# Kernel optimization log

Hardware: AMD Instinct MI355X
Metric: run time of the kernel (lower is better)

The kernel has to match this reference:

```python
import jax, jax.numpy as jnp
import numpy as np

B, L, D, Y = 8, 2500, 512, 8921


def setup_inputs() -> dict:
    key = jax.random.key(0)
    k1, k2, k3, k4, k5, k6 = jax.random.split(key, 6)
    x = jax.random.normal(k1, (B, L, D), dtype=jnp.float32)
    target = jax.random.uniform(k2, (B, Y), dtype=jnp.float32)
    text_inputs = jax.random.randint(k3, (B, L), 0, 50000, dtype=jnp.int32)
    # Xavier-uniform-like init for the two [Y, D] weights
    lim = float(np.sqrt(6.0 / (Y + D)))
    U_weight = jax.random.uniform(k4, (Y, D), dtype=jnp.float32, minval=-lim, maxval=lim)
    final_weight = jax.random.uniform(k5, (Y, D), dtype=jnp.float32, minval=-lim, maxval=lim)
    final_bias = jax.random.uniform(k6, (Y,), dtype=jnp.float32, minval=-0.05, maxval=0.05)
    return {"x": x, "target": target, "text_inputs": text_inputs,
            "U_weight": U_weight, "final_weight": final_weight, "final_bias": final_bias}


def reference(x, target, text_inputs, U_weight, final_weight, final_bias):
    # att: [B, Y, L] = U.weight @ x^T
    att = jnp.einsum('yd,bld->byl', U_weight, x)
    # softmax over sequence dim
    alpha = jax.nn.softmax(att, axis=2)
    # per-label context: [B, Y, D]
    m = jnp.einsum('byl,bld->byd', alpha, x)
    # gated reduction instead of a linear layer: [B, Y]
    y = jnp.einsum('byd,yd->by', m, final_weight) + final_bias
    # BCEWithLogitsLoss (mean over all elements), numerically stable
    loss = jnp.mean(jnp.maximum(y, 0.0) - y * target + jnp.log1p(jnp.exp(-jnp.abs(y))))
    return (y, loss)
```

## Files before the change

### kernel.cpp

```cpp
#include <hip/hip_runtime.h>
#include <stdint.h>

#define B_ 8
#define L_ 2500
#define D_ 512
#define Y_ 8921
#define LP 2560
#define YP 8960
#define BLK 128
#define BK 32
#define NKT 16
#define NS 4
#define LTS 5

typedef float f32x4 __attribute__((ext_vector_type(4)));
typedef __bf16 bf16x8 __attribute__((ext_vector_type(8)));
typedef unsigned short u16;
typedef unsigned int u32;

__device__ __forceinline__ u32 pack2(float a, float b) {
  u32 ua = __float_as_uint(a); ua = (ua + 0x7FFFu + ((ua >> 16) & 1u)) >> 16;
  u32 ub = __float_as_uint(b); ub = (ub + 0x7FFFu + ((ub >> 16) & 1u)) >> 16;
  return ua | (ub << 16);
}

__global__ void cvt_x_kernel(const float* __restrict__ x, u16* __restrict__ xb) {
  int idx = blockIdx.x * 256 + threadIdx.x;
  int row = idx >> 6;
  int c8  = (idx & 63) << 3;
  int b = row / LP;
  int l = row - b * LP;
  uint4 o;
  if (l < L_) {
    const float* s = x + (size_t)(b * L_ + l) * D_ + c8;
    float4 f0 = *(const float4*)s;
    float4 f1 = *(const float4*)(s + 4);
    o.x = pack2(f0.x, f0.y); o.y = pack2(f0.z, f0.w);
    o.z = pack2(f1.x, f1.y); o.w = pack2(f1.z, f1.w);
  } else {
    o = make_uint4(0u, 0u, 0u, 0u);
  }
  *(uint4*)(xb + (size_t)row * D_ + c8) = o;
}

__global__ void cvt_w_kernel(const float* __restrict__ U, const float* __restrict__ Wf,
                             u16* __restrict__ Ub, u16* __restrict__ Wb) {
  int idx = blockIdx.x * 256 + threadIdx.x;
  const int half = YP * 64;
  const float* src = U; u16* dst = Ub;
  int i = idx;
  if (idx >= half) { i -= half; src = Wf; dst = Wb; }
  int row = i >> 6;
  int c8  = (i & 63) << 3;
  uint4 o;
  if (row < Y_) {
    const float* s = src + (size_t)row * D_ + c8;
    float4 f0 = *(const float4*)s;
    float4 f1 = *(const float4*)(s + 4);
    o.x = pack2(f0.x, f0.y); o.y = pack2(f0.z, f0.w);
    o.z = pack2(f1.x, f1.y); o.w = pack2(f1.z, f1.w);
  } else {
    o = make_uint4(0u, 0u, 0u, 0u);
  }
  *(uint4*)(dst + (size_t)row * D_ + c8) = o;
}

__device__ __forceinline__ void async16(const u16* g, u16* l) {
  __builtin_amdgcn_global_load_lds(
      (const __attribute__((address_space(1))) u32*)g,
      (__attribute__((address_space(3))) u32*)l, 16, 0, 0);
}

__global__ __launch_bounds__(256, 2) void fused_kernel(
    const u16* __restrict__ xb,
    const u16* __restrict__ Ub,
    const u16* __restrict__ Wb,
    float* __restrict__ part)
{
  __shared__ __align__(16) u16 sU[BLK * BK];
  __shared__ __align__(16) u16 sW[BLK * BK];
  __shared__ __align__(16) u16 sX[BLK * BK];

  const int t    = threadIdx.x;
  const int lane = t & 63;
  const int wv   = t >> 6;
  const int l16  = lane & 15;
  const int q    = lane >> 4;
  const int b    = blockIdx.y;
  const int y0   = blockIdx.x * BLK;
  const int s    = blockIdx.z;

  const int srow = t >> 2;
  const int scol = (t & 3) << 3;
  const u16* gU0 = Ub + (size_t)(y0 + srow) * D_ + scol;
  const u16* gU1 = gU0 + (size_t)64 * D_;
  const u16* gW0 = Wb + (size_t)(y0 + srow) * D_ + scol;
  const u16* gW1 = gW0 + (size_t)64 * D_;
  const u16* gXb = xb + (size_t)b * LP * D_ + (size_t)srow * D_ + scol;
  u16* lU0 = sU + t * 8;  u16* lU1 = sU + 2048 + t * 8;
  u16* lW0 = sW + t * 8;  u16* lW1 = sW + 2048 + t * 8;
  u16* lX0 = sX + t * 8;  u16* lX1 = sX + 2048 + t * 8;

  float M[8], Z[8], W[8];
#pragma unroll
  for (int i = 0; i < 8; ++i) { M[i] = -1e30f; Z[i] = 0.f; W[i] = 0.f; }

  const f32x4 z4 = {0.f, 0.f, 0.f, 0.f};

  for (int ltl = 0; ltl < LTS; ++ltl) {
    const int l0 = (s * LTS + ltl) * BLK;
    const u16* gX0 = gXb + (size_t)l0 * D_;
    const u16* gX1 = gX0 + (size_t)64 * D_;

    f32x4 accA[2][8], accS[2][8];
#pragma unroll
    for (int ry = 0; ry < 2; ++ry)
#pragma unroll
      for (int cl = 0; cl < 8; ++cl) { accA[ry][cl] = z4; accS[ry][cl] = z4; }

    for (int kt = 0; kt < NKT; ++kt) {
      const int ko = kt * BK;
      __syncthreads();
      async16(gU0 + ko, lU0);
      async16(gU1 + ko, lU1);
      async16(gW0 + ko, lW0);
      async16(gW1 + ko, lW1);
      async16(gX0 + ko, lX0);
      async16(gX1 + ko, lX1);
      __syncthreads();

      bf16x8 aU0 = *(const bf16x8*)(const void*)(sU + (wv * 32 + l16) * BK + q * 8);
      bf16x8 aU1 = *(const bf16x8*)(const void*)(sU + (wv * 32 + 16 + l16) * BK + q * 8);
      bf16x8 aW0 = *(const bf16x8*)(const void*)(sW + (wv * 32 + l16) * BK + q * 8);
      bf16x8 aW1 = *(const bf16x8*)(const void*)(sW + (wv * 32 + 16 + l16) * BK + q * 8);
#pragma unroll
      for (int cl = 0; cl < 8; ++cl) {
        bf16x8 bX = *(const bf16x8*)(const void*)(sX + (cl * 16 + l16) * BK + q * 8);
        accA[0][cl] = __builtin_amdgcn_mfma_f32_16x16x32_bf16(aU0, bX, accA[0][cl], 0, 0, 0);
        accA[1][cl] = __builtin_amdgcn_mfma_f32_16x16x32_bf16(aU1, bX, accA[1][cl], 0, 0, 0);
        accS[0][cl] = __builtin_amdgcn_mfma_f32_16x16x32_bf16(aW0, bX, accS[0][cl], 0, 0, 0);
        accS[1][cl] = __builtin_amdgcn_mfma_f32_16x16x32_bf16(aW1, bX, accS[1][cl], 0, 0, 0);
      }
    }

    const bool boundary = (l0 + BLK > L_);
#pragma unroll
    for (int ry = 0; ry < 2; ++ry) {
#pragma unroll
      for (int r = 0; r < 4; ++r) {
        const int si = ry * 4 + r;
        float a[8];
        if (boundary) {
#pragma unroll
          for (int cl = 0; cl < 8; ++cl) {
            float v = accA[ry][cl][r];
            a[cl] = (l0 + cl * 16 + l16 >= L_) ? -1e30f : v;
          }
        } else {
#pragma unroll
          for (int cl = 0; cl < 8; ++cl) a[cl] = accA[ry][cl][r];
        }
        float tmax = a[0];
#pragma unroll
        for (int cl = 1; cl < 8; ++cl) tmax = fmaxf(tmax, a[cl]);
        const float mnew  = fmaxf(M[si], tmax);
        const float scale = __expf(M[si] - mnew);
        float zl = 0.f, wl = 0.f;
#pragma unroll
        for (int cl = 0; cl < 8; ++cl) {
          float p = __expf(a[cl] - mnew);
          zl += p;
          wl = fmaf(p, accS[ry][cl][r], wl);
        }
        Z[si] = fmaf(Z[si], scale, zl);
        W[si] = fmaf(W[si], scale, wl);
        M[si] = mnew;
      }
    }
  }

#pragma unroll
  for (int si = 0; si < 8; ++si) {
    float M0 = M[si], Z0 = Z[si], W0 = W[si];
#pragma unroll
    for (int st = 1; st <= 8; st <<= 1) {
      const float Mo = __shfl_xor(M0, st);
      const float Zo = __shfl_xor(Z0, st);
      const float Wo = __shfl_xor(W0, st);
      const float mn = fmaxf(M0, Mo);
      const float sa = __expf(M0 - mn);
      const float sb = __expf(Mo - mn);
      Z0 = Z0 * sa + Zo * sb;
      W0 = W0 * sa + Wo * sb;
      M0 = mn;
    }
    M[si] = M0; Z[si] = Z0; W[si] = W0;
  }

  if (l16 == 0) {
    float* p = part + ((size_t)(b * 70 + blockIdx.x) * NS + s) * 384;
#pragma unroll
    for (int ry = 0; ry < 2; ++ry) {
#pragma unroll
      for (int r = 0; r < 4; ++r) {
        const int si = ry * 4 + r;
        const int yl = wv * 32 + ry * 16 + q * 4 + r;
        p[yl]       = M[si];
        p[128 + yl] = Z[si];
        p[256 + yl] = W[si];
      }
    }
  }
}

__global__ void combine_kernel(const float* __restrict__ part,
                               const float* __restrict__ bias,
                               const float* __restrict__ target,
                               float* __restrict__ out) {
  const int idx = blockIdx.x * 256 + threadIdx.x;
  float lpart = 0.f;
  if (idx < B_ * Y_) {
    const int b = idx / Y_;
    const int y = idx - b * Y_;
    const int yt = y >> 7, yl = y & 127;
    const float* p = part + ((size_t)(b * 70 + yt) * NS) * 384 + yl;
    float M = -1e30f;
#pragma unroll
    for (int s2 = 0; s2 < NS; ++s2) M = fmaxf(M, p[s2 * 384]);
    float Z = 0.f, W = 0.f;
#pragma unroll
    for (int s2 = 0; s2 < NS; ++s2) {
      const float e = __expf(p[s2 * 384] - M);
      Z = fmaf(p[s2 * 384 + 128], e, Z);
      W = fmaf(p[s2 * 384 + 256], e, W);
    }
    const float yv = W / Z + bias[y];
    out[idx] = yv;
    const float tg = target[idx];
    lpart = fmaxf(yv, 0.f) - yv * tg + log1pf(__expf(-fabsf(yv)));
  }
  lpart += __shfl_xor(lpart, 1);  lpart += __shfl_xor(lpart, 2);
  lpart += __shfl_xor(lpart, 4);  lpart += __shfl_xor(lpart, 8);
  lpart += __shfl_xor(lpart, 16); lpart += __shfl_xor(lpart, 32);
  if ((threadIdx.x & 63) == 0)
    atomicAdd(out + (size_t)B_ * Y_, lpart * (1.0f / (B_ * Y_)));
}

extern "C" void kernel_launch(void* const* d_in, const int* in_sizes, int n_in,
                              void* d_out, int out_size, void* d_ws, size_t ws_size,
                              hipStream_t stream) {
  const float* x      = (const float*)d_in[0];
  const float* target = (const float*)d_in[1];
  const float* U      = (const float*)d_in[3];
  const float* Wf     = (const float*)d_in[4];
  const float* bias   = (const float*)d_in[5];
  float* out = (float*)d_out;

  u16* xb = (u16*)d_ws;
  u16* Ub = xb + (size_t)B_ * LP * D_;
  u16* Wb = Ub + (size_t)YP * D_;
  float* part = (float*)(Wb + (size_t)YP * D_);

  hipMemsetAsync(out + (size_t)B_ * Y_, 0, sizeof(float), stream);
  cvt_x_kernel<<<dim3((B_ * LP * 64) / 256), 256, 0, stream>>>(x, xb);
  cvt_w_kernel<<<dim3((2 * YP * 64) / 256), 256, 0, stream>>>(U, Wf, Ub, Wb);
  fused_kernel<<<dim3(YP / BLK, B_, NS), 256, 0, stream>>>(xb, Ub, Wb, part);
  combine_kernel<<<dim3((B_ * Y_ + 255) / 256), 256, 0, stream>>>(part, bias, target, out);
}
```

Baseline: 568.8 us.

## Switch fused attention GEMMs from bf16 to block-scaled MX-FP8 MFMA

Measured after the change: 2.070 ms. 3.64x slower.

```diff
diff --git a/kernel.cpp b/kernel.cpp
--- a/kernel.cpp
+++ b/kernel.cpp
@@ -8,78 +8,98 @@
 #define LP 2560
 #define YP 8960
 #define BLK 128
-#define BK 32
-#define NKT 16
 #define NS 4
 #define LTS 5
 
 typedef float f32x4 __attribute__((ext_vector_type(4)));
-typedef __bf16 bf16x8 __attribute__((ext_vector_type(8)));
-typedef unsigned short u16;
+typedef int   v8i  __attribute__((ext_vector_type(8)));
 typedef unsigned int u32;
-
-__device__ __forceinline__ u32 pack2(float a, float b) {
-  u32 ua = __float_as_uint(a); ua = (ua + 0x7FFFu + ((ua >> 16) & 1u)) >> 16;
-  u32 ub = __float_as_uint(b); ub = (ub + 0x7FFFu + ((ub >> 16) & 1u)) >> 16;
-  return ua | (ub << 16);
-}
-
-__global__ void cvt_x_kernel(const float* __restrict__ x, u16* __restrict__ xb) {
-  int idx = blockIdx.x * 256 + threadIdx.x;
-  int row = idx >> 6;
-  int c8  = (idx & 63) << 3;
-  int b = row / LP;
-  int l = row - b * LP;
-  uint4 o;
-  if (l < L_) {
-    const float* s = x + (size_t)(b * L_ + l) * D_ + c8;
-    float4 f0 = *(const float4*)s;
-    float4 f1 = *(const float4*)(s + 4);
-    o.x = pack2(f0.x, f0.y); o.y = pack2(f0.z, f0.w);
-    o.z = pack2(f1.x, f1.y); o.w = pack2(f1.z, f1.w);
+typedef uint8_t u8;
+
+__device__ __forceinline__ void quant32(const float* __restrict__ src, bool valid,
+                                        u8* __restrict__ dst, u8* __restrict__ sdst) {
+  float v[32];
+  float amax = 0.f;
+  if (valid) {
+#pragma unroll
+    for (int j = 0; j < 8; ++j) {
+      float4 f = *(const float4*)(src + j * 4);
+      v[j * 4 + 0] = f.x; v[j * 4 + 1] = f.y; v[j * 4 + 2] = f.z; v[j * 4 + 3] = f.w;
+      amax = fmaxf(amax, fmaxf(fmaxf(fabsf(f.x), fabsf(f.y)), fmaxf(fabsf(f.z), fabsf(f.w))));
+    }
   } else {
-    o = make_uint4(0u, 0u, 0u, 0u);
-  }
-  *(uint4*)(xb + (size_t)row * D_ + c8) = o;
-}
-
-__global__ void cvt_w_kernel(const float* __restrict__ U, const float* __restrict__ Wf,
-                             u16* __restrict__ Ub, u16* __restrict__ Wb) {
-  int idx = blockIdx.x * 256 + threadIdx.x;
-  const int half = YP * 64;
-  const float* src = U; u16* dst = Ub;
-  int i = idx;
-  if (idx >= half) { i -= half; src = Wf; dst = Wb; }
-  int row = i >> 6;
-  int c8  = (i & 63) << 3;
-  uint4 o;
-  if (row < Y_) {
-    const float* s = src + (size_t)row * D_ + c8;
-    float4 f0 = *(const float4*)s;
-    float4 f1 = *(const float4*)(s + 4);
-    o.x = pack2(f0.x, f0.y); o.y = pack2(f0.z, f0.w);
-    o.z = pack2(f1.x, f1.y); o.w = pack2(f1.z, f1.w);
-  } else {
-    o = make_uint4(0u, 0u, 0u, 0u);
-  }
-  *(uint4*)(dst + (size_t)row * D_ + c8) = o;
-}
-
-__device__ __forceinline__ void async16(const u16* g, u16* l) {
+#pragma unroll
+    for (int j = 0; j < 32; ++j) v[j] = 0.f;
+  }
+  int e = 0;
+  float sinv = 1.f;
+  if (amax > 0.f) {
+    e = (int)ceilf(__log2f(amax) - 8.80735492206f);
+    e = max(-127, min(127, e));
+    sinv = exp2f((float)(-e));
+  }
+  u32 w[8];
+#pragma unroll
+  for (int j = 0; j < 8; ++j) {
+    u32 r = __builtin_amdgcn_cvt_pk_fp8_f32(v[j * 4 + 0] * sinv, v[j * 4 + 1] * sinv, 0, false);
+    r = __builtin_amdgcn_cvt_pk_fp8_f32(v[j * 4 + 2] * sinv, v[j * 4 + 3] * sinv, r, true);
+    w[j] = r;
+  }
+  *(uint4*)dst        = make_uint4(w[0], w[1], w[2], w[3]);
+  *(uint4*)(dst + 16) = make_uint4(w[4], w[5], w[6], w[7]);
+  *sdst = (u8)(e + 127);
+}
+
+__global__ void cvt_x8(const float* __restrict__ x, u8* __restrict__ xb, u8* __restrict__ xs) {
+  int gid = blockIdx.x * 256 + threadIdx.x;
+  int row = gid >> 4, blk = gid & 15;
+  int b = row / LP, l = row - b * LP;
+  bool valid = (l < L_);
+  const float* src = x + (size_t)(b * L_ + l) * D_ + blk * 32;
+  quant32(src, valid, xb + (size_t)row * 512 + blk * 32, xs + (size_t)row * 16 + blk);
+}
+
+__global__ void cvt_w8(const float* __restrict__ U, const float* __restrict__ Wf,
+                       u8* __restrict__ Ub, u8* __restrict__ Us,
+                       u8* __restrict__ Wb, u8* __restrict__ Ws) {
+  int gid = blockIdx.x * 256 + threadIdx.x;
+  const int half = YP * 16;
+  const float* src = U; u8* db = Ub; u8* ds = Us;
+  int i = gid;
+  if (gid >= half) { i -= half; src = Wf; db = Wb; ds = Ws; }
+  int row = i >> 4, blk = i & 15;
+  bool valid = (row < Y_);
+  quant32(src + (size_t)row * D_ + blk * 32, valid,
+          db + (size_t)row * 512 + blk * 32, ds + (size_t)row * 16 + blk);
+}
+
+__device__ __forceinline__ void async16b(const u8* g, u8* l) {
   __builtin_amdgcn_global_load_lds(
       (const __attribute__((address_space(1))) u32*)g,
       (__attribute__((address_space(3))) u32*)l, 16, 0, 0);
 }
 
+__device__ __forceinline__ v8i ldfrag(const u8* s, int row, int q) {
+  const int h0 = (q * 2) ^ (row & 7);
+  const uint4 a = *(const uint4*)(s + row * 128 + h0 * 16);
+  const uint4 c = *(const uint4*)(s + row * 128 + (h0 ^ 1) * 16);
+  v8i r;
+  r[0] = a.x; r[1] = a.y; r[2] = a.z; r[3] = a.w;
+  r[4] = c.x; r[5] = c.y; r[6] = c.z; r[7] = c.w;
+  return r;
+}
+
 __global__ __launch_bounds__(256, 2) void fused_kernel(
-    const u16* __restrict__ xb,
-    const u16* __restrict__ Ub,
-    const u16* __restrict__ Wb,
+    const u8* __restrict__ xb, const u8* __restrict__ Ub, const u8* __restrict__ Wb,
+    const u8* __restrict__ Xs, const u8* __restrict__ Us, const u8* __restrict__ Ws,
     float* __restrict__ part)
 {
-  __shared__ __align__(16) u16 sU[BLK * BK];
-  __shared__ __align__(16) u16 sW[BLK * BK];
-  __shared__ __align__(16) u16 sX[BLK * BK];
+  __shared__ __align__(16) u8 sU[16384];
+  __shared__ __align__(16) u8 sW[16384];
+  __shared__ __align__(16) u8 sX[16384];
+  __shared__ __align__(16) u8 sUs[2048];
+  __shared__ __align__(16) u8 sWs[2048];
+  __shared__ __align__(16) u8 sXs[2048];
 
   const int t    = threadIdx.x;
   const int lane = t & 63;
@@ -90,16 +110,15 @@
   const int y0   = blockIdx.x * BLK;
   const int s    = blockIdx.z;
 
-  const int srow = t >> 2;
-  const int scol = (t & 3) << 3;
-  const u16* gU0 = Ub + (size_t)(y0 + srow) * D_ + scol;
-  const u16* gU1 = gU0 + (size_t)64 * D_;
-  const u16* gW0 = Wb + (size_t)(y0 + srow) * D_ + scol;
-  const u16* gW1 = gW0 + (size_t)64 * D_;
-  const u16* gXb = xb + (size_t)b * LP * D_ + (size_t)srow * D_ + scol;
-  u16* lU0 = sU + t * 8;  u16* lU1 = sU + 2048 + t * 8;
-  u16* lW0 = sW + t * 8;  u16* lW1 = sW + 2048 + t * 8;
-  u16* lX0 = sX + t * 8;  u16* lX1 = sX + 2048 + t * 8;
+  const int srow = t >> 3;
+  const int scol = (((t & 7) ^ (srow & 7)) << 4);
+  const u8* gU = Ub + (size_t)(y0 + srow) * 512 + scol;
+  const u8* gW = Wb + (size_t)(y0 + srow) * 512 + scol;
+  const u8* gXbase = xb + (size_t)b * LP * 512 + (size_t)srow * 512 + scol;
+  const u8* gXsc   = Xs + (size_t)b * LP * 16;
+
+  if (wv < 2) async16b(Us + (size_t)(y0 + t) * 16, sUs + t * 16);
+  else        async16b(Ws + (size_t)(y0 + (t - 128)) * 16, sWs + (t - 128) * 16);
 
   float M[8], Z[8], W[8];
 #pragma unroll
@@ -109,8 +128,7 @@
 
   for (int ltl = 0; ltl < LTS; ++ltl) {
     const int l0 = (s * LTS + ltl) * BLK;
-    const u16* gX0 = gXb + (size_t)l0 * D_;
-    const u16* gX1 = gX0 + (size_t)64 * D_;
+    const u8* gX = gXbase + (size_t)l0 * 512;
 
     f32x4 accA[2][8], accS[2][8];
 #pragma unroll
@@ -118,28 +136,38 @@
 #pragma unroll
       for (int cl = 0; cl < 8; ++cl) { accA[ry][cl] = z4; accS[ry][cl] = z4; }
 
-    for (int kt = 0; kt < NKT; ++kt) {
-      const int ko = kt * BK;
+    for (int kt = 0; kt < 4; ++kt) {
+      const int ko = kt * 128;
       __syncthreads();
-      async16(gU0 + ko, lU0);
-      async16(gU1 + ko, lU1);
-      async16(gW0 + ko, lW0);
-      async16(gW1 + ko, lW1);
-      async16(gX0 + ko, lX0);
-      async16(gX1 + ko, lX1);
+      if (kt == 0 && t < 128)
+        async16b(gXsc + (size_t)(l0 + t) * 16, sXs + t * 16);
+#pragma unroll
+      for (int r = 0; r < 4; ++r) {
+        async16b(gU + ko + (size_t)r * 32 * 512, sU + r * 4096 + t * 16);
+        async16b(gW + ko + (size_t)r * 32 * 512, sW + r * 4096 + t * 16);
+        async16b(gX + ko + (size_t)r * 32 * 512, sX + r * 4096 + t * 16);
+      }
       __syncthreads();
 
-      bf16x8 aU0 = *(const bf16x8*)(const void*)(sU + (wv * 32 + l16) * BK + q * 8);
-      bf16x8 aU1 = *(const bf16x8*)(const void*)(sU + (wv * 32 + 16 + l16) * BK + q * 8);
-      bf16x8 aW0 = *(const bf16x8*)(const void*)(sW + (wv * 32 + l16) * BK + q * 8);
-      bf16x8 aW1 = *(const bf16x8*)(const void*)(sW + (wv * 32 + 16 + l16) * BK + q * 8);
+      const int r0 = wv * 32 + l16;
+      const int sh = q * 8;
+      v8i aU0 = ldfrag(sU, r0, q);
+      v8i aU1 = ldfrag(sU, r0 + 16, q);
+      v8i aW0 = ldfrag(sW, r0, q);
+      v8i aW1 = ldfrag(sW, r0 + 16, q);
+      int scU0 = (int)(*(const u32*)(sUs + r0 * 16 + kt * 4) >> sh);
+      int scU1 = (int)(*(const u32*)(sUs + (r0 + 16) * 16 + kt * 4) >> sh);
+      int scW0 = (int)(*(const u32*)(sWs + r0 * 16 + kt * 4) >> sh);
+      int scW1 = (int)(*(const u32*)(sWs + (r0 + 16) * 16 + kt * 4) >> sh);
 #pragma unroll
       for (int cl = 0; cl < 8; ++cl) {
-        bf16x8 bX = *(const bf16x8*)(const void*)(sX + (cl * 16 + l16) * BK + q * 8);
-        accA[0][cl] = __builtin_amdgcn_mfma_f32_16x16x32_bf16(aU0, bX, accA[0][cl], 0, 0, 0);
-        accA[1][cl] = __builtin_amdgcn_mfma_f32_16x16x32_bf16(aU1, bX, accA[1][cl], 0, 0, 0);
-        accS[0][cl] = __builtin_amdgcn_mfma_f32_16x16x32_bf16(aW0, bX, accS[0][cl], 0, 0, 0);
-        accS[1][cl] = __builtin_amdgcn_mfma_f32_16x16x32_bf16(aW1, bX, accS[1][cl], 0, 0, 0);
+        const int rb = cl * 16 + l16;
+        v8i bX = ldfrag(sX, rb, q);
+        int scX = (int)(*(const u32*)(sXs + rb * 16 + kt * 4) >> sh);
+        accA[0][cl] = __builtin_amdgcn_mfma_scale_f32_16x16x128_f8f6f4(aU0, bX, accA[0][cl], 0, 0, 0, scU0, 0, scX);
+        accA[1][cl] = __builtin_amdgcn_mfma_scale_f32_16x16x128_f8f6f4(aU1, bX, accA[1][cl], 0, 0, 0, scU1, 0, scX);
+        accS[0][cl] = __builtin_amdgcn_mfma_scale_f32_16x16x128_f8f6f4(aW0, bX, accS[0][cl], 0, 0, 0, scW0, 0, scX);
+        accS[1][cl] = __builtin_amdgcn_mfma_scale_f32_16x16x128_f8f6f4(aW1, bX, accS[1][cl], 0, 0, 0, scW1, 0, scX);
       }
     }
 
@@ -256,14 +284,17 @@
   const float* bias   = (const float*)d_in[5];
   float* out = (float*)d_out;
 
-  u16* xb = (u16*)d_ws;
-  u16* Ub = xb + (size_t)B_ * LP * D_;
-  u16* Wb = Ub + (size_t)YP * D_;
-  float* part = (float*)(Wb + (size_t)YP * D_);
+  u8* xb  = (u8*)d_ws;
+  u8* Ub8 = xb + (size_t)B_ * LP * 512;
+  u8* Wb8 = Ub8 + (size_t)YP * 512;
+  u8* Xs  = Wb8 + (size_t)YP * 512;
+  u8* Us8 = Xs + (size_t)B_ * LP * 16;
+  u8* Ws8 = Us8 + (size_t)YP * 16;
+  float* part = (float*)(Ws8 + (size_t)YP * 16);
 
   hipMemsetAsync(out + (size_t)B_ * Y_, 0, sizeof(float), stream);
-  cvt_x_kernel<<<dim3((B_ * LP * 64) / 256), 256, 0, stream>>>(x, xb);
-  cvt_w_kernel<<<dim3((2 * YP * 64) / 256), 256, 0, stream>>>(U, Wf, Ub, Wb);
-  fused_kernel<<<dim3(YP / BLK, B_, NS), 256, 0, stream>>>(xb, Ub, Wb, part);
+  cvt_x8<<<dim3((B_ * LP * 16) / 256), 256, 0, stream>>>(x, xb, Xs);
+  cvt_w8<<<dim3((2 * YP * 16) / 256), 256, 0, stream>>>(U, Wf, Ub8, Us8, Wb8, Ws8);
+  fused_kernel<<<dim3(YP / BLK, B_, NS), 256, 0, stream>>>(xb, Ub8, Wb8, Xs, Us8, Ws8, part);
   combine_kernel<<<dim3((B_ * Y_ + 255) / 256), 256, 0, stream>>>(part, bias, target, out);
 }
```
